# Kernel tuning notes

Measured on AMD Instinct MI355X. Metric: run time of the kernel, lower is better.

The kernel has to match this reference:

```python
import jax, jax.numpy as jnp
import numpy as np

BONES = [(0, 1), (0, 2), (1, 3), (2, 4), (0, 5), (0, 6), (5, 7), (7, 9), (6, 8),
         (8, 10), (5, 11), (6, 12), (11, 13), (13, 15), (12, 14), (14, 16)]
NUM_JOINTS = 17


def _adjacency():
    a = np.zeros((NUM_JOINTS, NUM_JOINTS), dtype=np.float32)
    for i, j in BONES:
        a[i, j] = 1.0
        a[j, i] = 1.0
    a += np.eye(NUM_JOINTS, dtype=np.float32)  # adj + I, no normalization (matches source)
    return jnp.asarray(a)


def _xavier(key, shape):
    fan_in, fan_out = shape
    lim = float(np.sqrt(6.0 / (fan_in + fan_out)))
    return jax.random.uniform(key, shape, jnp.float32, -lim, lim)


def setup_inputs() -> dict:
    key = jax.random.key(0)
    ks = jax.random.split(key, 4)
    B, T, J, D_in, H, D_out = 128, 512, NUM_JOINTS, 2, 64, 32
    x = jax.random.normal(ks[0], (B, T, J, D_in), dtype=jnp.float32)
    return {
        "x": x,
        "W1": _xavier(ks[1], (D_in, H)), "b1": jnp.zeros((H,), jnp.float32),
        "W2": _xavier(ks[2], (H, H)),    "b2": jnp.zeros((H,), jnp.float32),
        "W3": _xavier(ks[3], (H, D_out)),"b3": jnp.zeros((D_out,), jnp.float32),
        "adj": _adjacency(),
    }


def _gc(x, adj, W, b):
    # support = x @ W ; out = adj @ support + b, batched over (B, T)
    support = jnp.einsum('btjd,df->btjf', x, W)
    return jnp.einsum('ij,btjf->btif', adj, support) + b


def reference(x, W1, b1, W2, b2, W3, b3, adj):
    # Dropout is identity in eval mode (p=0.1 train-only in the source).
    h = jax.nn.relu(_gc(x, adj, W1, b1))
    h = jax.nn.relu(_gc(h, adj, W2, b2))
    return _gc(h, adj, W3, b3)  # [B, T, 17, 32]
```

## Files before the change

kernel.cpp:

```cpp
#include <hip/hip_runtime.h>
#include <hip/hip_bf16.h>


#define NJ 17
#define TB 4
#define RPAD 80
#define HD 64
#define DOUT 32
#define LDH 72

typedef __attribute__((ext_vector_type(8))) short bf16x8;
typedef __attribute__((ext_vector_type(4))) float f32x4;
typedef __attribute__((ext_vector_type(2))) float f32x2;

__device__ __forceinline__ unsigned pkbf(float a, float b) {
    __hip_bfloat162 h = __float22bfloat162_rn(make_float2(a, b));
    union { __hip_bfloat162 h; unsigned u; } c; c.h = h; return c.u;
}

#define PK2(a,b)       (2u | ((a)<<3) | ((b)<<8))
#define PK3(a,b,c)     (3u | ((a)<<3) | ((b)<<8) | ((c)<<13))
#define PK4(a,b,c,d)   (4u | ((a)<<3) | ((b)<<8) | ((c)<<13) | ((d)<<18))
#define PK5(a,b,c,d,e) (5u | ((a)<<3) | ((b)<<8) | ((c)<<13) | ((d)<<18) | ((e)<<23))
__constant__ unsigned ADJP[NJ] = {
    PK5(0,1,2,5,6), PK3(1,0,3),    PK3(2,0,4),    PK2(3,1),       PK2(4,2),
    PK4(5,0,7,11),  PK4(6,0,8,12), PK3(7,5,9),    PK3(8,6,10),    PK2(9,7),
    PK2(10,8),      PK3(11,5,13),  PK3(12,6,14),  PK3(13,11,15),  PK3(14,12,16),
    PK2(15,13),     PK2(16,14)
};

#define GRAPH_APPLY(H, A) \
    H[0]=A(0)+A(1)+A(2)+A(5)+A(6); \
    H[1]=A(1)+A(0)+A(3); \
    H[2]=A(2)+A(0)+A(4); \
    H[3]=A(3)+A(1); \
    H[4]=A(4)+A(2); \
    H[5]=A(5)+A(0)+A(7)+A(11); \
    H[6]=A(6)+A(0)+A(8)+A(12); \
    H[7]=A(7)+A(5)+A(9); \
    H[8]=A(8)+A(6)+A(10); \
    H[9]=A(9)+A(7); \
    H[10]=A(10)+A(8); \
    H[11]=A(11)+A(5)+A(13); \
    H[12]=A(12)+A(6)+A(14); \
    H[13]=A(13)+A(11)+A(15); \
    H[14]=A(14)+A(12)+A(16); \
    H[15]=A(15)+A(13); \
    H[16]=A(16)+A(14);

__device__ __forceinline__ bf16x8 load_bfrag(const float* __restrict__ W, int ncols,
                                             int n, int kb) {
    const float* p = W + (size_t)kb * ncols + n;
    union { unsigned u[4]; bf16x8 v; } r;
    #pragma unroll
    for (int e = 0; e < 4; ++e)
        r.u[e] = pkbf(p[(2 * e) * ncols], p[(2 * e + 1) * ncols]);
    return r.v;
}

__global__ __launch_bounds__(256, 4)
void sge_fused(const float* __restrict__ x,
               const float* __restrict__ W1, const float* __restrict__ b1,
               const float* __restrict__ W2, const float* __restrict__ b2,
               const float* __restrict__ W3, const float* __restrict__ b3,
               float* __restrict__ out)
{
    __shared__ __align__(16) short h2buf[RPAD * LDH];
    __shared__ __align__(8)  float zs[RPAD * 2];

    const int tid = threadIdx.x;
    const int btBase = blockIdx.x * TB;

    if (tid < RPAD * 2) {
        int r = tid >> 1, d = tid & 1;
        int g = (r >> 2) & 3, j = (r >> 4) * 4 + (r & 3);
        float s = 0.f;
        if (j < NJ) {
            unsigned p = ADJP[j];
            int cnt = p & 7u; p >>= 3;
            const float* xb = x + (size_t)(btBase + g) * (NJ * 2) + d;
            for (int c = 0; c < cnt; ++c) { s += xb[(p & 31u) * 2]; p >>= 5; }
        }
        zs[tid] = s;
    }
    __syncthreads();

    const int lane = tid & 63, wave = tid >> 6;
    const int lm = lane & 15, lq = lane >> 4;
    const int k0 = lq * 8;

    f32x2 zv[5];
    #pragma unroll
    for (int mt = 0; mt < 5; ++mt)
        zv[mt] = *(const f32x2*)&zs[(mt * 16 + lm) * 2];

    f32x4 acc[5];
    #pragma unroll
    for (int mt = 0; mt < 5; ++mt) acc[mt] = (f32x4){0.f, 0.f, 0.f, 0.f};

    #pragma unroll
    for (int f = 0; f < 2; ++f) {
        const int kb = f * 32 + k0;
        const float4 wa0 = *(const float4*)&W1[kb];
        const float4 wa1 = *(const float4*)&W1[kb + 4];
        const float4 wb0 = *(const float4*)&W1[HD + kb];
        const float4 wb1 = *(const float4*)&W1[HD + kb + 4];
        const float4 bv0 = *(const float4*)&b1[kb];
        const float4 bv1 = *(const float4*)&b1[kb + 4];
        const bf16x8 bfr = load_bfrag(W2, HD, wave * 16 + lm, kb);
        #pragma unroll
        for (int mt = 0; mt < 5; ++mt) {
            const float z0 = zv[mt][0], z1 = zv[mt][1];
            float h0 = fmaxf(fmaf(z0, wa0.x, fmaf(z1, wb0.x, bv0.x)), 0.f);
            float h1 = fmaxf(fmaf(z0, wa0.y, fmaf(z1, wb0.y, bv0.y)), 0.f);
            float h2 = fmaxf(fmaf(z0, wa0.z, fmaf(z1, wb0.z, bv0.z)), 0.f);
            float h3 = fmaxf(fmaf(z0, wa0.w, fmaf(z1, wb0.w, bv0.w)), 0.f);
            float h4 = fmaxf(fmaf(z0, wa1.x, fmaf(z1, wb1.x, bv1.x)), 0.f);
            float h5 = fmaxf(fmaf(z0, wa1.y, fmaf(z1, wb1.y, bv1.y)), 0.f);
            float h6 = fmaxf(fmaf(z0, wa1.z, fmaf(z1, wb1.z, bv1.z)), 0.f);
            float h7 = fmaxf(fmaf(z0, wa1.w, fmaf(z1, wb1.w, bv1.w)), 0.f);
            union { unsigned u[4]; bf16x8 v; } af;
            af.u[0] = pkbf(h0, h1); af.u[1] = pkbf(h2, h3);
            af.u[2] = pkbf(h4, h5); af.u[3] = pkbf(h6, h7);
            acc[mt] = __builtin_amdgcn_mfma_f32_16x16x32_bf16(af.v, bfr, acc[mt], 0, 0, 0);
        }
    }

    {
        const int c = wave * 16 + lm;
        const float b2c = b2[c];
        float hv[17];
        #define A2(j) acc[(j) >> 2][(j) & 3]
        GRAPH_APPLY(hv, A2)
        #undef A2
        short* hw = &h2buf[lq * 4 * LDH + c];
        #pragma unroll
        for (int j = 0; j < 17; ++j)
            hw[(((j >> 2) * 16) + (j & 3)) * LDH] =
                (short)pkbf(fmaxf(hv[j] + b2c, 0.f), 0.f);
    }
    __syncthreads();

    if (wave < 2) {
        const bf16x8 w3f0 = load_bfrag(W3, DOUT, wave * 16 + lm, k0);
        const bf16x8 w3f1 = load_bfrag(W3, DOUT, wave * 16 + lm, 32 + k0);
        f32x4 a3[5];
        #pragma unroll
        for (int mt = 0; mt < 5; ++mt) a3[mt] = (f32x4){0.f, 0.f, 0.f, 0.f};
        const short* hr = &h2buf[lm * LDH + k0];
        #pragma unroll
        for (int mt = 0; mt < 5; ++mt) {
            bf16x8 a0 = *(const bf16x8*)&hr[mt * 16 * LDH];
            bf16x8 a1 = *(const bf16x8*)&hr[mt * 16 * LDH + 32];
            a3[mt] = __builtin_amdgcn_mfma_f32_16x16x32_bf16(a0, w3f0, a3[mt], 0, 0, 0);
            a3[mt] = __builtin_amdgcn_mfma_f32_16x16x32_bf16(a1, w3f1, a3[mt], 0, 0, 0);
        }
        const float b3c = b3[wave * 16 + lm];
        float ov[17];
        #define A3(j) a3[(j) >> 2][(j) & 3]
        GRAPH_APPLY(ov, A3)
        #undef A3
        float* og = out + (size_t)(btBase + lq) * (NJ * DOUT) + wave * 16 + lm;
        #pragma unroll
        for (int j = 0; j < 17; ++j)
            og[j * DOUT] = ov[j] + b3c;
    }
}

extern "C" void kernel_launch(void* const* d_in, const int* in_sizes, int n_in,
                              void* d_out, int out_size, void* d_ws, size_t ws_size,
                              hipStream_t stream) {
    const float* x  = (const float*)d_in[0];
    const float* W1 = (const float*)d_in[1];
    const float* b1 = (const float*)d_in[2];
    const float* W2 = (const float*)d_in[3];
    const float* b2 = (const float*)d_in[4];
    const float* W3 = (const float*)d_in[5];
    const float* b3 = (const float*)d_in[6];
    float* out = (float*)d_out;

    const int nbt = in_sizes[0] / (NJ * 2);
    hipLaunchKernelGGL(sge_fused, dim3(nbt / TB), dim3(256), 0, stream,
                       x, W1, b1, W2, b2, W3, b3, out);
}
```

Before: 212.2 us.

## Process eight frames per block and stage layer-1 output through LDS

```diff
diff --git a/kernel.cpp b/kernel.cpp
--- a/kernel.cpp
+++ b/kernel.cpp
@@ -3,20 +3,21 @@
 
 
 #define NJ 17
-#define TB 4
-#define RPAD 80
+#define TB 8
+#define NT 10
+#define NR 160
 #define HD 64
 #define DOUT 32
 #define LDH 72
 
 typedef __attribute__((ext_vector_type(8))) short bf16x8;
 typedef __attribute__((ext_vector_type(4))) float f32x4;
-typedef __attribute__((ext_vector_type(2))) float f32x2;
 
 __device__ __forceinline__ unsigned pkbf(float a, float b) {
     __hip_bfloat162 h = __float22bfloat162_rn(make_float2(a, b));
     union { __hip_bfloat162 h; unsigned u; } c; c.h = h; return c.u;
 }
+__device__ __forceinline__ short bf16s(float v) { return (short)pkbf(v, v); }
 
 #define PK2(a,b)       (2u | ((a)<<3) | ((b)<<8))
 #define PK3(a,b,c)     (3u | ((a)<<3) | ((b)<<8) | ((c)<<13))
@@ -58,22 +59,28 @@
     return r.v;
 }
 
-__global__ __launch_bounds__(256, 4)
+__global__ __launch_bounds__(256, 6)
 void sge_fused(const float* __restrict__ x,
                const float* __restrict__ W1, const float* __restrict__ b1,
                const float* __restrict__ W2, const float* __restrict__ b2,
                const float* __restrict__ W3, const float* __restrict__ b3,
                float* __restrict__ out)
 {
-    __shared__ __align__(16) short h2buf[RPAD * LDH];
-    __shared__ __align__(8)  float zs[RPAD * 2];
+    __shared__ __align__(16) short hbuf[NR * LDH];
+    __shared__ __align__(8)  float zs[NR * 2];
 
     const int tid = threadIdx.x;
     const int btBase = blockIdx.x * TB;
-
-    if (tid < RPAD * 2) {
-        int r = tid >> 1, d = tid & 1;
-        int g = (r >> 2) & 3, j = (r >> 4) * 4 + (r & 3);
+    const int lane = tid & 63, wave = tid >> 6;
+    const int lm = lane & 15, lq = lane >> 4;
+    const int k0 = lq * 8;
+
+    for (int i = tid; i < NR * 2; i += 256) {
+        int r = i >> 1, d = i & 1;
+        int h = (r >= 80) ? 1 : 0;
+        int rp = r - 80 * h;
+        int j = (rp >> 4) * 4 + (rp & 3);
+        int g = 4 * h + ((rp >> 2) & 3);
         float s = 0.f;
         if (j < NJ) {
             unsigned p = ADJP[j];
@@ -81,73 +88,84 @@
             const float* xb = x + (size_t)(btBase + g) * (NJ * 2) + d;
             for (int c = 0; c < cnt; ++c) { s += xb[(p & 31u) * 2]; p >>= 5; }
         }
-        zs[tid] = s;
-    }
-    __syncthreads();
-
-    const int lane = tid & 63, wave = tid >> 6;
-    const int lm = lane & 15, lq = lane >> 4;
-    const int k0 = lq * 8;
-
-    f32x2 zv[5];
+        zs[i] = s;
+    }
+    __syncthreads();
+
+    {
+        const int ko = tid & 7;
+        const int f0 = ko * 8;
+        const int r0 = tid >> 3;
+        const float4 wa0 = *(const float4*)&W1[f0];
+        const float4 wa1 = *(const float4*)&W1[f0 + 4];
+        const float4 wb0 = *(const float4*)&W1[HD + f0];
+        const float4 wb1 = *(const float4*)&W1[HD + f0 + 4];
+        const float4 bv0 = *(const float4*)&b1[f0];
+        const float4 bv1 = *(const float4*)&b1[f0 + 4];
+        #pragma unroll
+        for (int it = 0; it < 5; ++it) {
+            const int r = r0 + 32 * it;
+            const float z0 = zs[2 * r], z1 = zs[2 * r + 1];
+            float v0 = fmaxf(fmaf(z0, wa0.x, fmaf(z1, wb0.x, bv0.x)), 0.f);
+            float v1 = fmaxf(fmaf(z0, wa0.y, fmaf(z1, wb0.y, bv0.y)), 0.f);
+            float v2 = fmaxf(fmaf(z0, wa0.z, fmaf(z1, wb0.z, bv0.z)), 0.f);
+            float v3 = fmaxf(fmaf(z0, wa0.w, fmaf(z1, wb0.w, bv0.w)), 0.f);
+            float v4 = fmaxf(fmaf(z0, wa1.x, fmaf(z1, wb1.x, bv1.x)), 0.f);
+            float v5 = fmaxf(fmaf(z0, wa1.y, fmaf(z1, wb1.y, bv1.y)), 0.f);
+            float v6 = fmaxf(fmaf(z0, wa1.z, fmaf(z1, wb1.z, bv1.z)), 0.f);
+            float v7 = fmaxf(fmaf(z0, wa1.w, fmaf(z1, wb1.w, bv1.w)), 0.f);
+            *(uint4*)&hbuf[r * LDH + f0] =
+                make_uint4(pkbf(v0, v1), pkbf(v2, v3), pkbf(v4, v5), pkbf(v6, v7));
+        }
+    }
+    __syncthreads();
+
+    const int cw = wave * 16 + lm;
+    f32x4 acc[NT];
     #pragma unroll
-    for (int mt = 0; mt < 5; ++mt)
-        zv[mt] = *(const f32x2*)&zs[(mt * 16 + lm) * 2];
-
-    f32x4 acc[5];
-    #pragma unroll
-    for (int mt = 0; mt < 5; ++mt) acc[mt] = (f32x4){0.f, 0.f, 0.f, 0.f};
-
-    #pragma unroll
-    for (int f = 0; f < 2; ++f) {
-        const int kb = f * 32 + k0;
-        const float4 wa0 = *(const float4*)&W1[kb];
-        const float4 wa1 = *(const float4*)&W1[kb + 4];
-        const float4 wb0 = *(const float4*)&W1[HD + kb];
-        const float4 wb1 = *(const float4*)&W1[HD + kb + 4];
-        const float4 bv0 = *(const float4*)&b1[kb];
-        const float4 bv1 = *(const float4*)&b1[kb + 4];
-        const bf16x8 bfr = load_bfrag(W2, HD, wave * 16 + lm, kb);
-        #pragma unroll
-        for (int mt = 0; mt < 5; ++mt) {
-            const float z0 = zv[mt][0], z1 = zv[mt][1];
-            float h0 = fmaxf(fmaf(z0, wa0.x, fmaf(z1, wb0.x, bv0.x)), 0.f);
-            float h1 = fmaxf(fmaf(z0, wa0.y, fmaf(z1, wb0.y, bv0.y)), 0.f);
-            float h2 = fmaxf(fmaf(z0, wa0.z, fmaf(z1, wb0.z, bv0.z)), 0.f);
-            float h3 = fmaxf(fmaf(z0, wa0.w, fmaf(z1, wb0.w, bv0.w)), 0.f);
-            float h4 = fmaxf(fmaf(z0, wa1.x, fmaf(z1, wb1.x, bv1.x)), 0.f);
-            float h5 = fmaxf(fmaf(z0, wa1.y, fmaf(z1, wb1.y, bv1.y)), 0.f);
-            float h6 = fmaxf(fmaf(z0, wa1.z, fmaf(z1, wb1.z, bv1.z)), 0.f);
-            float h7 = fmaxf(fmaf(z0, wa1.w, fmaf(z1, wb1.w, bv1.w)), 0.f);
-            union { unsigned u[4]; bf16x8 v; } af;
-            af.u[0] = pkbf(h0, h1); af.u[1] = pkbf(h2, h3);
-            af.u[2] = pkbf(h4, h5); af.u[3] = pkbf(h6, h7);
-            acc[mt] = __builtin_amdgcn_mfma_f32_16x16x32_bf16(af.v, bfr, acc[mt], 0, 0, 0);
-        }
-    }
-
-    {
-        const int c = wave * 16 + lm;
-        const float b2c = b2[c];
-        float hv[17];
-        #define A2(j) acc[(j) >> 2][(j) & 3]
-        GRAPH_APPLY(hv, A2)
-        #undef A2
-        short* hw = &h2buf[lq * 4 * LDH + c];
-        #pragma unroll
-        for (int j = 0; j < 17; ++j)
-            hw[(((j >> 2) * 16) + (j & 3)) * LDH] =
-                (short)pkbf(fmaxf(hv[j] + b2c, 0.f), 0.f);
-    }
-    __syncthreads();
-
-    if (wave < 2) {
-        const bf16x8 w3f0 = load_bfrag(W3, DOUT, wave * 16 + lm, k0);
-        const bf16x8 w3f1 = load_bfrag(W3, DOUT, wave * 16 + lm, 32 + k0);
+    for (int mt = 0; mt < NT; ++mt) acc[mt] = (f32x4){0.f, 0.f, 0.f, 0.f};
+    {
+        const bf16x8 bk0 = load_bfrag(W2, HD, cw, k0);
+        const bf16x8 bk1 = load_bfrag(W2, HD, cw, 32 + k0);
+        const short* ar = &hbuf[lm * LDH + k0];
+        #pragma unroll
+        for (int mt = 0; mt < NT; ++mt) {
+            bf16x8 a0 = *(const bf16x8*)&ar[mt * 16 * LDH];
+            bf16x8 a1 = *(const bf16x8*)&ar[mt * 16 * LDH + 32];
+            acc[mt] = __builtin_amdgcn_mfma_f32_16x16x32_bf16(a0, bk0, acc[mt], 0, 0, 0);
+            acc[mt] = __builtin_amdgcn_mfma_f32_16x16x32_bf16(a1, bk1, acc[mt], 0, 0, 0);
+        }
+    }
+    __syncthreads();
+
+    {
+        const float b2c = b2[cw];
+        short* hw = &hbuf[lq * 4 * LDH + cw];
+        float hv[NJ];
+        #define AL(j) acc[(j) >> 2][(j) & 3]
+        GRAPH_APPLY(hv, AL)
+        #undef AL
+        #pragma unroll
+        for (int j = 0; j < NJ; ++j)
+            hw[(((j >> 2) * 16) + (j & 3)) * LDH] = bf16s(fmaxf(hv[j] + b2c, 0.f));
+        #define AH(j) acc[5 + ((j) >> 2)][(j) & 3]
+        GRAPH_APPLY(hv, AH)
+        #undef AH
+        #pragma unroll
+        for (int j = 0; j < NJ; ++j)
+            hw[(80 + ((j >> 2) * 16) + (j & 3)) * LDH] = bf16s(fmaxf(hv[j] + b2c, 0.f));
+    }
+    __syncthreads();
+
+    {
+        const int pr = wave >> 1;
+        const int c3 = (wave & 1) * 16 + lm;
+        const bf16x8 w3f0 = load_bfrag(W3, DOUT, c3, k0);
+        const bf16x8 w3f1 = load_bfrag(W3, DOUT, c3, 32 + k0);
         f32x4 a3[5];
         #pragma unroll
         for (int mt = 0; mt < 5; ++mt) a3[mt] = (f32x4){0.f, 0.f, 0.f, 0.f};
-        const short* hr = &h2buf[lm * LDH + k0];
+        const short* hr = &hbuf[(pr * 80 + lm) * LDH + k0];
         #pragma unroll
         for (int mt = 0; mt < 5; ++mt) {
             bf16x8 a0 = *(const bf16x8*)&hr[mt * 16 * LDH];
@@ -155,14 +173,14 @@
             a3[mt] = __builtin_amdgcn_mfma_f32_16x16x32_bf16(a0, w3f0, a3[mt], 0, 0, 0);
             a3[mt] = __builtin_amdgcn_mfma_f32_16x16x32_bf16(a1, w3f1, a3[mt], 0, 0, 0);
         }
-        const float b3c = b3[wave * 16 + lm];
-        float ov[17];
+        const float b3c = b3[c3];
+        float ov[NJ];
         #define A3(j) a3[(j) >> 2][(j) & 3]
         GRAPH_APPLY(ov, A3)
         #undef A3
-        float* og = out + (size_t)(btBase + lq) * (NJ * DOUT) + wave * 16 + lm;
-        #pragma unroll
-        for (int j = 0; j < 17; ++j)
+        float* og = out + (size_t)(btBase + 4 * pr + lq) * (NJ * DOUT) + c3;
+        #pragma unroll
+        for (int j = 0; j < NJ; ++j)
             og[j * DOUT] = ov[j] + b3c;
     }
 }
```

Result: faster. 190.9 us (-10.0%).
